# Kernel optimization log

Measured on AMD Instinct MI355X. Metric: run time of the kernel, lower is better.

Reference implementation:

```python
import jax, jax.numpy as jnp
import numpy as np
import math

C = 128
LAM = 0.25
MARGIN = 0.3
TAU = math.log(C)
B = 8192


def lambertw(z, iters=10):
    """Principal-branch Lambert W via Halley iterations (valid for z >= -1/e)."""
    e = jnp.exp(1.0)
    # series init near the branch point z = -1/e, log init for z >= 0
    p = jnp.sqrt(jnp.maximum(2.0 * (e * z + 1.0), 0.0))
    w_near = -1.0 + p - p * p / 3.0 + (11.0 / 72.0) * p ** 3
    w = jnp.where(z < 0.0, w_near, jnp.log1p(jnp.maximum(z, 0.0)))
    for _ in range(iters):
        ew = jnp.exp(w)
        f = w * ew - z
        wp1 = w + 1.0
        w = w - f / (ew * wp1 - (w + 2.0) * f / (2.0 * wp1))
    return w


def triplet_loss(x, targets):
    # pairwise euclidean distances [B, B]
    sq = jnp.sum(x * x, axis=1)
    dist = sq[:, None] + sq[None, :] - 2.0 * (x @ x.T)
    dist = jnp.sqrt(jnp.maximum(dist, 1e-12))
    pos = targets[:, None] == targets[None, :]
    # hardest positive / hardest negative per anchor
    dist_ap = jnp.max(jnp.where(pos, dist, -jnp.inf), axis=1)
    dist_an = jnp.min(jnp.where(pos, jnp.inf, dist), axis=1)
    # MarginRankingLoss(margin)(dist_an, dist_ap, y=1), mean reduction
    return jnp.mean(jnp.maximum(dist_ap - dist_an + MARGIN, 0.0))


def cross_entropy(logits, targets):
    logp = jax.nn.log_softmax(logits, axis=-1)
    return -jnp.mean(jnp.take_along_axis(logp, targets[:, None], axis=1)[:, 0])


def setup_inputs() -> dict:
    key = jax.random.key(0)
    k1, k2 = jax.random.split(key)
    logits = jax.random.normal(k1, (B, C), dtype=jnp.float32)
    targets = jax.random.randint(k2, (B,), 0, C, dtype=jnp.int64)
    return {"logits": logits, "targets": targets}


def reference(logits, targets):
    # l_i is detached in the original (and sigma goes through numpy -> no grad)
    l_i = jax.lax.stop_gradient(triplet_loss(logits, targets))
    y = 0.5 * jnp.maximum(-2.0 / jnp.exp(1.0), (l_i - TAU) / LAM)
    sigma = jax.lax.stop_gradient(jnp.exp(-lambertw(y)))
    ce = cross_entropy(logits, targets)
    loss = (ce - TAU) * sigma + LAM * jnp.log(sigma) ** 2
    return jnp.sum(loss) / B
```

## Files before the change

kernel.cpp:

```cpp
#include <hip/hip_runtime.h>
#include <math.h>

#define NB 8192
#define NC 128
#define NJS 8
#define JPT 8

typedef short v8s __attribute__((ext_vector_type(8)));
typedef float v4f __attribute__((ext_vector_type(4)));

__device__ inline unsigned bf16rne(float f) {
    unsigned u = __float_as_uint(f);
    return (u + 0x7fffu + ((u >> 16) & 1u)) >> 16;
}

__global__ __launch_bounds__(256) void k_prep(const float* __restrict__ x,
                                              const int* __restrict__ tgt,
                                              unsigned* __restrict__ xb,
                                              float* __restrict__ sq,
                                              float* __restrict__ ce,
                                              unsigned* __restrict__ gmax,
                                              unsigned* __restrict__ gmin) {
    int row = blockIdx.x * 4 + (threadIdx.x >> 6);
    int l = threadIdx.x & 63;
    float2 v = ((const float2*)(x + row * NC))[l];
    xb[row * 64 + l] = bf16rne(v.x) | (bf16rne(v.y) << 16);
    float ss = fmaf(v.x, v.x, v.y * v.y);
    float mx = fmaxf(v.x, v.y);
#pragma unroll
    for (int off = 32; off; off >>= 1) {
        ss += __shfl_xor(ss, off);
        mx = fmaxf(mx, __shfl_xor(mx, off));
    }
    float es = expf(v.x - mx) + expf(v.y - mx);
#pragma unroll
    for (int off = 32; off; off >>= 1) es += __shfl_xor(es, off);
    if (l == 0) {
        sq[row] = ss;
        ce[row] = mx + logf(es) - x[row * NC + tgt[row]];
        gmax[row] = 0u;
        gmin[row] = 0x7f800000u;
    }
}

__global__ __launch_bounds__(256, 2) void k_trip(const unsigned* __restrict__ xb,
                                                 const int* __restrict__ tgt,
                                                 const float* __restrict__ sq,
                                                 unsigned* __restrict__ gmax,
                                                 unsigned* __restrict__ gmin) {
    __shared__ short As[128 * 128];
    __shared__ short Bs[128 * 128];
    const int tid = threadIdx.x;
    const int lane = tid & 63;
    const int w = tid >> 6;
    const int rh = w >> 1;
    const int ch = w & 1;
    const int i0 = blockIdx.x * 128;

#pragma unroll
    for (int c = 0; c < 8; ++c) {
        int L = w * 512 + c * 64 + lane;
        int r = L >> 4, cc = L & 15;
        const unsigned* src = xb + (size_t)(i0 + r) * 64 + (((cc ^ (r & 7)) << 2));
        __builtin_amdgcn_global_load_lds(
            (const __attribute__((address_space(1))) unsigned*)src,
            (__attribute__((address_space(3))) unsigned*)(As + (w * 512 + c * 64) * 8),
            16, 0, 0);
    }

    int ti[4][4];
#pragma unroll
    for (int tm = 0; tm < 4; ++tm)
#pragma unroll
        for (int r = 0; r < 4; ++r) {
            int rowloc = rh * 64 + tm * 16 + ((lane >> 4) << 2) + r;
            ti[tm][r] = tgt[i0 + rowloc];
        }

    float mp[4][4], mn[4][4];
#pragma unroll
    for (int tm = 0; tm < 4; ++tm)
#pragma unroll
        for (int r = 0; r < 4; ++r) { mp[tm][r] = -3.0e38f; mn[tm][r] = 3.0e38f; }

    for (int jt = 0; jt < JPT; ++jt) {
        int j0 = (blockIdx.y * JPT + jt) * 128;
        __syncthreads();
#pragma unroll
        for (int c = 0; c < 8; ++c) {
            int L = w * 512 + c * 64 + lane;
            int r = L >> 4, cc = L & 15;
            const unsigned* src = xb + (size_t)(j0 + r) * 64 + (((cc ^ (r & 7)) << 2));
            __builtin_amdgcn_global_load_lds(
                (const __attribute__((address_space(1))) unsigned*)src,
                (__attribute__((address_space(3))) unsigned*)(Bs + (w * 512 + c * 64) * 8),
                16, 0, 0);
        }
        __syncthreads();

        v4f acc[4][4];
        v4f z = {0.0f, 0.0f, 0.0f, 0.0f};
#pragma unroll
        for (int tm = 0; tm < 4; ++tm)
#pragma unroll
            for (int tn = 0; tn < 4; ++tn) acc[tm][tn] = z;

        const int m = lane & 15;
        const int quad = lane >> 4;
#pragma unroll
        for (int ks = 0; ks < 4; ++ks) {
            v8s a[4], b[4];
            int q = ks * 4 + quad;
#pragma unroll
            for (int tm = 0; tm < 4; ++tm) {
                int row = rh * 64 + tm * 16 + m;
                a[tm] = *(const v8s*)(As + row * 128 + ((q ^ (row & 7)) << 3));
            }
#pragma unroll
            for (int tn = 0; tn < 4; ++tn) {
                int col = ch * 64 + tn * 16 + m;
                b[tn] = *(const v8s*)(Bs + col * 128 + ((q ^ (col & 7)) << 3));
            }
#pragma unroll
            for (int tm = 0; tm < 4; ++tm)
#pragma unroll
                for (int tn = 0; tn < 4; ++tn)
                    acc[tm][tn] = __builtin_amdgcn_mfma_f32_16x16x32_bf16(
                        a[tm], b[tn], acc[tm][tn], 0, 0, 0);
        }

#pragma unroll
        for (int tn = 0; tn < 4; ++tn) {
            int col = j0 + ch * 64 + tn * 16 + m;
            float sqj = sq[col];
            int tj = tgt[col];
#pragma unroll
            for (int tm = 0; tm < 4; ++tm)
#pragma unroll
                for (int r = 0; r < 4; ++r) {
                    float v = fmaf(-2.0f, acc[tm][tn][r], sqj);
                    bool pos = (tj == ti[tm][r]);
                    mp[tm][r] = fmaxf(mp[tm][r], pos ? v : -3.0e38f);
                    mn[tm][r] = fminf(mn[tm][r], pos ? 3.0e38f : v);
                }
        }
    }

#pragma unroll
    for (int off = 1; off < 16; off <<= 1) {
#pragma unroll
        for (int tm = 0; tm < 4; ++tm)
#pragma unroll
            for (int r = 0; r < 4; ++r) {
                mp[tm][r] = fmaxf(mp[tm][r], __shfl_xor(mp[tm][r], off));
                mn[tm][r] = fminf(mn[tm][r], __shfl_xor(mn[tm][r], off));
            }
    }
    if ((lane & 15) == 0) {
#pragma unroll
        for (int tm = 0; tm < 4; ++tm)
#pragma unroll
            for (int r = 0; r < 4; ++r) {
                int i = i0 + rh * 64 + tm * 16 + ((lane >> 4) << 2) + r;
                float s = sq[i];
                float d2p = fmaxf(s + mp[tm][r], 0.0f);
                float d2n = fmaxf(s + mn[tm][r], 0.0f);
                atomicMax(gmax + i, __float_as_uint(d2p));
                atomicMin(gmin + i, __float_as_uint(d2n));
            }
    }
}

__global__ __launch_bounds__(1024) void k_tail(const unsigned* __restrict__ gmax,
                                               const unsigned* __restrict__ gmin,
                                               const float* __restrict__ ce,
                                               float* __restrict__ out) {
    float hs = 0.0f, cs = 0.0f;
    for (int i = threadIdx.x; i < NB; i += 1024) {
        float ap = sqrtf(fmaxf(__uint_as_float(gmax[i]), 1e-12f));
        float an = sqrtf(fmaxf(__uint_as_float(gmin[i]), 1e-12f));
        hs += fmaxf(ap - an + 0.3f, 0.0f);
        cs += ce[i];
    }
#pragma unroll
    for (int off = 32; off; off >>= 1) {
        hs += __shfl_xor(hs, off);
        cs += __shfl_xor(cs, off);
    }
    __shared__ float sh[16], sc[16];
    int wv = threadIdx.x >> 6;
    if ((threadIdx.x & 63) == 0) { sh[wv] = hs; sc[wv] = cs; }
    __syncthreads();
    if (threadIdx.x == 0) {
        double H = 0.0, Cs = 0.0;
        for (int k = 0; k < 16; ++k) { H += sh[k]; Cs += sc[k]; }
        const double E = 2.71828182845904523536;
        const double TAU = log(128.0);
        const double LAMd = 0.25;
        double l = H / (double)NB;
        double cev = Cs / (double)NB;
        double y = 0.5 * fmax(-2.0 / E, (l - TAU) / LAMd);
        double p = sqrt(fmax(2.0 * (E * y + 1.0), 0.0));
        double wn = -1.0 + p - p * p / 3.0 + (11.0 / 72.0) * p * p * p;
        double wlw = (y < 0.0) ? wn : log1p(fmax(y, 0.0));
#pragma unroll
        for (int it = 0; it < 10; ++it) {
            double ew = exp(wlw);
            double f = wlw * ew - y;
            double wp1 = wlw + 1.0;
            wlw = wlw - f / (ew * wp1 - (wlw + 2.0) * f / (2.0 * wp1));
        }
        double sigma = exp(-wlw);
        double lg = log(sigma);
        double loss = (cev - TAU) * sigma + LAMd * lg * lg;
        out[0] = (float)(loss / (double)NB);
    }
}

extern "C" void kernel_launch(void* const* d_in, const int* in_sizes, int n_in,
                              void* d_out, int out_size, void* d_ws, size_t ws_size,
                              hipStream_t stream) {
    const float* x = (const float*)d_in[0];
    const int* tgt = (const int*)d_in[1];
    float* out = (float*)d_out;

    unsigned* xb = (unsigned*)d_ws;
    float* sq = (float*)(xb + (size_t)NB * 64);
    float* ce = sq + NB;
    unsigned* gmax = (unsigned*)(ce + NB);
    unsigned* gmin = gmax + NB;

    k_prep<<<NB / 4, 256, 0, stream>>>(x, tgt, xb, sq, ce, gmax, gmin);
    dim3 grid(NB / 128, NJS);
    k_trip<<<grid, 256, 0, stream>>>(xb, tgt, sq, gmax, gmin);
    k_tail<<<1, 1024, 0, stream>>>(gmax, gmin, ce, out);
}
```

Measured before the change: 93.76 us.

## Double-buffer B tiles, keep A fragments in registers, fuse tail via last-block counter

```diff
diff --git a/kernel.cpp b/kernel.cpp
--- a/kernel.cpp
+++ b/kernel.cpp
@@ -20,7 +20,8 @@
                                               float* __restrict__ sq,
                                               float* __restrict__ ce,
                                               unsigned* __restrict__ gmax,
-                                              unsigned* __restrict__ gmin) {
+                                              unsigned* __restrict__ gmin,
+                                              unsigned* __restrict__ cnt) {
     int row = blockIdx.x * 4 + (threadIdx.x >> 6);
     int l = threadIdx.x & 63;
     float2 v = ((const float2*)(x + row * NC))[l];
@@ -41,41 +42,57 @@
         gmax[row] = 0u;
         gmin[row] = 0x7f800000u;
     }
+    if (blockIdx.x == 0 && threadIdx.x == 0) *cnt = 0u;
 }
 
 __global__ __launch_bounds__(256, 2) void k_trip(const unsigned* __restrict__ xb,
                                                  const int* __restrict__ tgt,
                                                  const float* __restrict__ sq,
                                                  unsigned* __restrict__ gmax,
-                                                 unsigned* __restrict__ gmin) {
-    __shared__ short As[128 * 128];
-    __shared__ short Bs[128 * 128];
+                                                 unsigned* __restrict__ gmin,
+                                                 const float* __restrict__ ce,
+                                                 unsigned* __restrict__ cnt,
+                                                 float* __restrict__ out) {
+    __shared__ short Bs[2][128 * 128];
+    __shared__ float sh[4], sc2[4];
+    __shared__ unsigned lastFlag;
+
     const int tid = threadIdx.x;
     const int lane = tid & 63;
     const int w = tid >> 6;
     const int rh = w >> 1;
     const int ch = w & 1;
     const int i0 = blockIdx.x * 128;
+    const int jbase = blockIdx.y * JPT * 128;
+    const int m = lane & 15;
+    const int quad = lane >> 4;
 
 #pragma unroll
     for (int c = 0; c < 8; ++c) {
         int L = w * 512 + c * 64 + lane;
         int r = L >> 4, cc = L & 15;
-        const unsigned* src = xb + (size_t)(i0 + r) * 64 + (((cc ^ (r & 7)) << 2));
+        const unsigned* src = xb + (size_t)(jbase + r) * 64 + ((cc ^ (r & 7)) << 2);
         __builtin_amdgcn_global_load_lds(
             (const __attribute__((address_space(1))) unsigned*)src,
-            (__attribute__((address_space(3))) unsigned*)(As + (w * 512 + c * 64) * 8),
+            (__attribute__((address_space(3))) unsigned*)(&Bs[0][0] + (w * 512 + c * 64) * 8),
             16, 0, 0);
     }
 
+    v8s a[4][4];
+#pragma unroll
+    for (int tm = 0; tm < 4; ++tm)
+#pragma unroll
+        for (int ks = 0; ks < 4; ++ks) {
+            int row = i0 + rh * 64 + tm * 16 + m;
+            a[tm][ks] = *(const v8s*)(xb + (size_t)row * 64 + (ks * 4 + quad) * 4);
+        }
+
     int ti[4][4];
 #pragma unroll
     for (int tm = 0; tm < 4; ++tm)
 #pragma unroll
-        for (int r = 0; r < 4; ++r) {
-            int rowloc = rh * 64 + tm * 16 + ((lane >> 4) << 2) + r;
-            ti[tm][r] = tgt[i0 + rowloc];
-        }
+        for (int r = 0; r < 4; ++r)
+            ti[tm][r] = tgt[i0 + rh * 64 + tm * 16 + quad * 4 + r];
 
     float mp[4][4], mn[4][4];
 #pragma unroll
@@ -83,20 +100,34 @@
 #pragma unroll
         for (int r = 0; r < 4; ++r) { mp[tm][r] = -3.0e38f; mn[tm][r] = 3.0e38f; }
 
+    __syncthreads();
+
     for (int jt = 0; jt < JPT; ++jt) {
-        int j0 = (blockIdx.y * JPT + jt) * 128;
-        __syncthreads();
-#pragma unroll
-        for (int c = 0; c < 8; ++c) {
-            int L = w * 512 + c * 64 + lane;
-            int r = L >> 4, cc = L & 15;
-            const unsigned* src = xb + (size_t)(j0 + r) * 64 + (((cc ^ (r & 7)) << 2));
-            __builtin_amdgcn_global_load_lds(
-                (const __attribute__((address_space(1))) unsigned*)src,
-                (__attribute__((address_space(3))) unsigned*)(Bs + (w * 512 + c * 64) * 8),
-                16, 0, 0);
-        }
-        __syncthreads();
+        int j0 = jbase + jt * 128;
+        const short* Bcur = &Bs[jt & 1][0];
+
+        if (jt + 1 < JPT) {
+            int jn = j0 + 128;
+            short* Bnxt = &Bs[(jt + 1) & 1][0];
+#pragma unroll
+            for (int c = 0; c < 8; ++c) {
+                int L = w * 512 + c * 64 + lane;
+                int r = L >> 4, cc = L & 15;
+                const unsigned* src = xb + (size_t)(jn + r) * 64 + ((cc ^ (r & 7)) << 2);
+                __builtin_amdgcn_global_load_lds(
+                    (const __attribute__((address_space(1))) unsigned*)src,
+                    (__attribute__((address_space(3))) unsigned*)(Bnxt + (w * 512 + c * 64) * 8),
+                    16, 0, 0);
+            }
+        }
+
+        float sqj[4]; int tj[4];
+#pragma unroll
+        for (int tn = 0; tn < 4; ++tn) {
+            int col = j0 + ch * 64 + tn * 16 + m;
+            sqj[tn] = sq[col];
+            tj[tn] = tgt[col];
+        }
 
         v4f acc[4][4];
         v4f z = {0.0f, 0.0f, 0.0f, 0.0f};
@@ -105,45 +136,37 @@
 #pragma unroll
             for (int tn = 0; tn < 4; ++tn) acc[tm][tn] = z;
 
-        const int m = lane & 15;
-        const int quad = lane >> 4;
 #pragma unroll
         for (int ks = 0; ks < 4; ++ks) {
-            v8s a[4], b[4];
+            v8s b[4];
             int q = ks * 4 + quad;
-#pragma unroll
-            for (int tm = 0; tm < 4; ++tm) {
-                int row = rh * 64 + tm * 16 + m;
-                a[tm] = *(const v8s*)(As + row * 128 + ((q ^ (row & 7)) << 3));
-            }
 #pragma unroll
             for (int tn = 0; tn < 4; ++tn) {
                 int col = ch * 64 + tn * 16 + m;
-                b[tn] = *(const v8s*)(Bs + col * 128 + ((q ^ (col & 7)) << 3));
+                b[tn] = *(const v8s*)(Bcur + col * 128 + ((q ^ (col & 7)) << 3));
             }
 #pragma unroll
             for (int tm = 0; tm < 4; ++tm)
 #pragma unroll
                 for (int tn = 0; tn < 4; ++tn)
                     acc[tm][tn] = __builtin_amdgcn_mfma_f32_16x16x32_bf16(
-                        a[tm], b[tn], acc[tm][tn], 0, 0, 0);
+                        a[tm][ks], b[tn], acc[tm][tn], 0, 0, 0);
         }
 
 #pragma unroll
         for (int tn = 0; tn < 4; ++tn) {
-            int col = j0 + ch * 64 + tn * 16 + m;
-            float sqj = sq[col];
-            int tj = tgt[col];
 #pragma unroll
             for (int tm = 0; tm < 4; ++tm)
 #pragma unroll
                 for (int r = 0; r < 4; ++r) {
-                    float v = fmaf(-2.0f, acc[tm][tn][r], sqj);
-                    bool pos = (tj == ti[tm][r]);
+                    float v = fmaf(-2.0f, acc[tm][tn][r], sqj[tn]);
+                    bool pos = (tj[tn] == ti[tm][r]);
                     mp[tm][r] = fmaxf(mp[tm][r], pos ? v : -3.0e38f);
                     mn[tm][r] = fminf(mn[tm][r], pos ? 3.0e38f : v);
                 }
         }
+
+        __syncthreads();
     }
 
 #pragma unroll
@@ -156,12 +179,12 @@
                 mn[tm][r] = fminf(mn[tm][r], __shfl_xor(mn[tm][r], off));
             }
     }
-    if ((lane & 15) == 0) {
+    if (m == 0) {
 #pragma unroll
         for (int tm = 0; tm < 4; ++tm)
 #pragma unroll
             for (int r = 0; r < 4; ++r) {
-                int i = i0 + rh * 64 + tm * 16 + ((lane >> 4) << 2) + r;
+                int i = i0 + rh * 64 + tm * 16 + quad * 4 + r;
                 float s = sq[i];
                 float d2p = fmaxf(s + mp[tm][r], 0.0f);
                 float d2n = fmaxf(s + mn[tm][r], 0.0f);
@@ -169,16 +192,21 @@
                 atomicMin(gmin + i, __float_as_uint(d2n));
             }
     }
-}
-
-__global__ __launch_bounds__(1024) void k_tail(const unsigned* __restrict__ gmax,
-                                               const unsigned* __restrict__ gmin,
-                                               const float* __restrict__ ce,
-                                               float* __restrict__ out) {
+
+    __threadfence();
+    if (tid == 0) {
+        unsigned prev = atomicAdd(cnt, 1u);
+        lastFlag = (prev == (unsigned)(gridDim.x * gridDim.y - 1));
+    }
+    __syncthreads();
+    if (!lastFlag) return;
+
     float hs = 0.0f, cs = 0.0f;
-    for (int i = threadIdx.x; i < NB; i += 1024) {
-        float ap = sqrtf(fmaxf(__uint_as_float(gmax[i]), 1e-12f));
-        float an = sqrtf(fmaxf(__uint_as_float(gmin[i]), 1e-12f));
+    for (int i = tid; i < NB; i += 256) {
+        unsigned up = atomicMax(gmax + i, 0u);
+        unsigned un = atomicMin(gmin + i, 0x7f800000u);
+        float ap = sqrtf(fmaxf(__uint_as_float(up), 1e-12f));
+        float an = sqrtf(fmaxf(__uint_as_float(un), 1e-12f));
         hs += fmaxf(ap - an + 0.3f, 0.0f);
         cs += ce[i];
     }
@@ -187,13 +215,11 @@
         hs += __shfl_xor(hs, off);
         cs += __shfl_xor(cs, off);
     }
-    __shared__ float sh[16], sc[16];
-    int wv = threadIdx.x >> 6;
-    if ((threadIdx.x & 63) == 0) { sh[wv] = hs; sc[wv] = cs; }
+    if (lane == 0) { sh[w] = hs; sc2[w] = cs; }
     __syncthreads();
-    if (threadIdx.x == 0) {
+    if (tid == 0) {
         double H = 0.0, Cs = 0.0;
-        for (int k = 0; k < 16; ++k) { H += sh[k]; Cs += sc[k]; }
+        for (int k = 0; k < 4; ++k) { H += sh[k]; Cs += sc2[k]; }
         const double E = 2.71828182845904523536;
         const double TAU = log(128.0);
         const double LAMd = 0.25;
@@ -229,9 +255,9 @@
     float* ce = sq + NB;
     unsigned* gmax = (unsigned*)(ce + NB);
     unsigned* gmin = gmax + NB;
-
-    k_prep<<<NB / 4, 256, 0, stream>>>(x, tgt, xb, sq, ce, gmax, gmin);
+    unsigned* cnt = gmin + NB;
+
+    k_prep<<<NB / 4, 256, 0, stream>>>(x, tgt, xb, sq, ce, gmax, gmin, cnt);
     dim3 grid(NB / 128, NJS);
-    k_trip<<<grid, 256, 0, stream>>>(xb, tgt, sq, gmax, gmin);
-    k_tail<<<1, 1024, 0, stream>>>(gmax, gmin, ce, out);
-}
+    k_trip<<<grid, 256, 0, stream>>>(xb, tgt, sq, gmax, gmin, ce, cnt, out);
+}
```

Result: slower. 146.2 us (+55.9%).
